# Kernel tuning notes

Measured on AMD Instinct MI355X. Metric: run time of the kernel, lower is better.

Reference implementation:

```python
import jax, jax.numpy as jnp
import numpy as np

D, H, L, NE, B, S, VOCAB = 512, 8, 4, 8, 32, 512, 64
HD = D // H
NEG = -1e9


def setup_inputs() -> dict:
    keys = iter(jax.random.split(jax.random.key(0), 64))
    def n(shape, s=0.02):
        return jax.random.normal(next(keys), shape, dtype=jnp.float32) * s
    return dict(
        x_batch=jax.random.randint(next(keys), (B, S), 0, VOCAB),
        context_batch=jax.random.normal(next(keys), (B, 2), dtype=jnp.float32),
        specialist_ids=jax.random.randint(next(keys), (B,), 0, NE),
        emb=n((VOCAB, D), 1.0),
        Wq=n((L, D, D)), bq=jnp.zeros((L, D)),
        Wk=n((L, D, D)), bk=jnp.zeros((L, D)),
        Wv=n((L, D, D)), bv=jnp.zeros((L, D)),
        Wo=n((L, D, D)), bo=jnp.zeros((L, D)),
        ln1_s=jnp.ones((L, D)), ln1_b=jnp.zeros((L, D)),
        ln2_s=jnp.ones((L, D)), ln2_b=jnp.zeros((L, D)),
        W1=n((L, D, 4 * D)), b1=jnp.zeros((L, 4 * D)),
        W2=n((L, 4 * D, D)), b2=jnp.zeros((L, D)),
        ctxW=n((2, D), 0.5), ctxb=jnp.zeros((D,)),
        cWq=n((D, D)), cbq=jnp.zeros((D,)),
        cWk=n((D, D)), cbk=jnp.zeros((D,)),
        cWv=n((D, D)), cbv=jnp.zeros((D,)),
        cWo=n((D, D)), cbo=jnp.zeros((D,)),
        spWp=n((NE, D, 64)), spbp=jnp.zeros((NE, 64)),
        spWa=n((NE, D, 64)), spba=jnp.zeros((NE, 64)),
    )


def _ln(x, s, b, eps=1e-5):
    m = x.mean(-1, keepdims=True)
    v = ((x - m) ** 2).mean(-1, keepdims=True)
    return (x - m) / jnp.sqrt(v + eps) * s + b


def _mha(q_in, kv_in, wq, bq_, wk, bk_, wv, bv_, wo, bo_, bias=None):
    # batch_first MultiheadAttention, H heads of dim HD
    Bq, Sq, _ = q_in.shape
    Sk = kv_in.shape[1]
    q = (q_in @ wq + bq_).reshape(Bq, Sq, H, HD).transpose(0, 2, 1, 3)
    k = (kv_in @ wk + bk_).reshape(Bq, Sk, H, HD).transpose(0, 2, 1, 3)
    v = (kv_in @ wv + bv_).reshape(Bq, Sk, H, HD).transpose(0, 2, 1, 3)
    scores = jnp.einsum('bhqd,bhkd->bhqk', q, k) / jnp.sqrt(jnp.float32(HD))
    if bias is not None:
        scores = scores + bias
    p = jax.nn.softmax(scores, axis=-1)
    o = jnp.einsum('bhqk,bhkd->bhqd', p, v).transpose(0, 2, 1, 3).reshape(Bq, Sq, D)
    return o @ wo + bo_


def reference(x_batch, context_batch, specialist_ids, emb, Wq, bq, Wk, bk, Wv, bv, Wo, bo,
              ln1_s, ln1_b, ln2_s, ln2_b, W1, b1, W2, b2, ctxW, ctxb,
              cWq, cbq, cWk, cbk, cWv, cbv, cWo, cbo, spWp, spbp, spWa, spba):
    x = emb[x_batch]  # [B,S,D]
    causal = jnp.where(jnp.tril(jnp.ones((S, S), dtype=bool)), 0.0, NEG)[None, None]
    # post-norm TransformerEncoderLayer (torch default): attn -> add+LN -> FFN(relu) -> add+LN
    for l in range(L):
        a = _mha(x, x, Wq[l], bq[l], Wk[l], bk[l], Wv[l], bv[l], Wo[l], bo[l], bias=causal)
        x = _ln(x + a, ln1_s[l], ln1_b[l])
        f = jax.nn.relu(x @ W1[l] + b1[l]) @ W2[l] + b2[l]
        x = _ln(x + f, ln2_s[l], ln2_b[l])
    ctx = (context_batch @ ctxW + ctxb)[:, None, :]  # [B,1,D]
    x = _mha(x, ctx, cWq, cbq, cWk, cbk, cWv, cbv, cWo, cbo)  # cross-attn, kv_len=1
    last = x[:, -1, :]  # [B,D]
    # expert routing: gather per-example expert params (equivalent to boolean-mask loop)
    pred = jnp.einsum('bd,bdo->bo', last, spWp[specialist_ids]) + spbp[specialist_ids]
    act = jnp.einsum('bd,bdo->bo', last, spWa[specialist_ids]) + spba[specialist_ids]
    return pred, act
```

## Files before the change

### kernel.cpp

```cpp
#include <hip/hip_runtime.h>


#define DD 512

__global__ __launch_bounds__(512) void stage_gemv3(
    const float* __restrict__ x0, const float* __restrict__ x1,
    const float* __restrict__ x2,
    const float* __restrict__ W,
    const float* __restrict__ bias2,
    float*       __restrict__ dst)
{
    __shared__ float sx[3 * DD];
    __shared__ float red[32][48];
    const int t = threadIdx.x;
    const int cbase = blockIdx.x * 16;

    if (t < DD) {
        sx[t]          = x0[t];
        sx[DD + t]     = x1[t];
        sx[2 * DD + t] = x2[t];
    }
    __syncthreads();

    const int c = t & 15, dg = t >> 4;
    const float* wp = W + (size_t)(dg * 16) * DD + cbase + c;
    float wreg[16];
    #pragma unroll
    for (int j = 0; j < 16; ++j)
        wreg[j] = wp[(size_t)j * DD];
    float p0 = 0.f, p1 = 0.f, p2 = 0.f;
    #pragma unroll
    for (int j = 0; j < 16; ++j) {
        const int d = dg * 16 + j;
        p0 += sx[d] * wreg[j];
        p1 += sx[DD + d] * wreg[j];
        p2 += sx[2 * DD + d] * wreg[j];
    }
    red[dg][c * 3 + 0] = p0;
    red[dg][c * 3 + 1] = p1;
    red[dg][c * 3 + 2] = p2;
    __syncthreads();

    if (t < 48) {
        const int cc = t / 3, vec = t % 3;
        float s = 0.f;
        #pragma unroll
        for (int g = 0; g < 32; ++g) s += red[g][t];
        if (vec == 2) s += bias2[cbase + cc];
        dst[vec * DD + cbase + cc] = s;
    }
}

__global__ __launch_bounds__(256) void stage_heads(
    const float* __restrict__ Bv,
    const float* __restrict__ spWp, const float* __restrict__ spbp,
    const float* __restrict__ spWa, const float* __restrict__ spba,
    const float* __restrict__ ctxin,
    const int*   __restrict__ sid,
    float*       __restrict__ out)
{
    __shared__ float sb[3 * DD];
    __shared__ float red[16][48];
    __shared__ float pv[48];
    __shared__ float sc0[32], sc1[32];
    __shared__ int   ssid[32];
    const int t = threadIdx.x;
    const int s = blockIdx.x & 7, h = (blockIdx.x >> 3) & 1, q = blockIdx.x >> 4;

    for (int i = t; i < 3 * DD; i += 256) sb[i] = Bv[i];
    if (t < 32) {
        ssid[t] = sid[t];
        sc0[t] = ctxin[2 * t];
        sc1[t] = ctxin[2 * t + 1];
    }
    __syncthreads();

    const float* W    = (h ? spWa : spWp) + (size_t)s * DD * 64;
    const float* bias = (h ? spba : spbp) + s * 64;
    const int o16 = t & 15, dg = t >> 4;
    const int o = q * 16 + o16;
    const float* wp = W + (size_t)(dg * 32) * 64 + o;
    float wreg[32];
    #pragma unroll
    for (int j = 0; j < 32; ++j)
        wreg[j] = wp[(size_t)j * 64];
    float p0 = 0.f, p1 = 0.f, p2 = 0.f;
    #pragma unroll
    for (int j = 0; j < 32; ++j) {
        const int d = dg * 32 + j;
        p0 += sb[d] * wreg[j];
        p1 += sb[DD + d] * wreg[j];
        p2 += sb[2 * DD + d] * wreg[j];
    }
    red[dg][o16 * 3 + 0] = p0;
    red[dg][o16 * 3 + 1] = p1;
    red[dg][o16 * 3 + 2] = p2;
    __syncthreads();

    if (t < 48) {
        const int oo = t / 3, vec = t % 3;
        float a = 0.f;
        #pragma unroll
        for (int g = 0; g < 16; ++g) a += red[g][t];
        if (vec == 2) a += bias[q * 16 + oo];
        pv[oo * 3 + vec] = a;
    }
    __syncthreads();

    if (t < 16) {
        const float v0 = pv[t * 3], v1 = pv[t * 3 + 1], v2 = pv[t * 3 + 2];
        #pragma unroll
        for (int b = 0; b < 32; ++b) {
            if (ssid[b] == s) {
                out[h * 2048 + b * 64 + q * 16 + t] =
                    sc0[b] * v0 + sc1[b] * v1 + v2;
            }
        }
    }
}

extern "C" void kernel_launch(void* const* d_in, const int* in_sizes, int n_in,
                              void* d_out, int out_size, void* d_ws, size_t ws_size,
                              hipStream_t stream) {
    const float* ctxin = (const float*)d_in[1];
    const int*   sid   = (const int*)d_in[2];
    const float* ctxW  = (const float*)d_in[20];
    const float* ctxb  = (const float*)d_in[21];
    const float* cWv   = (const float*)d_in[26];
    const float* cbv   = (const float*)d_in[27];
    const float* cWo   = (const float*)d_in[28];
    const float* cbo   = (const float*)d_in[29];
    const float* spWp  = (const float*)d_in[30];
    const float* spbp  = (const float*)d_in[31];
    const float* spWa  = (const float*)d_in[32];
    const float* spba  = (const float*)d_in[33];
    float* out = (float*)d_out;
    float* wsA = (float*)d_ws;
    float* wsB = wsA + 3 * DD;

    stage_gemv3<<<dim3(32), dim3(512), 0, stream>>>(
        ctxW, ctxW + DD, ctxb, cWv, cbv, wsA);
    stage_gemv3<<<dim3(32), dim3(512), 0, stream>>>(
        wsA, wsA + DD, wsA + 2 * DD, cWo, cbo, wsB);
    stage_heads<<<dim3(64), dim3(256), 0, stream>>>(
        wsB, spWp, spbp, spWa, spba, ctxin, sid, out);
}
```

Before: 152.3 us.

## Fuse three GEMV stages into one kernel with atomic accumulation and spin-wait

Replaces the three-kernel chain (value projection, output projection, expert heads) with one launch. Producer blocks compute the value projection and immediately apply their slice of the output projection, accumulating into a zeroed workspace with atomics and signalling a counter. Consumer blocks preload expert weights, spin on the counter, then finish the heads. This removes two kernel launches and lets weight loads overlap, at the cost of an extra memset, atomic contention, and reliance on all blocks being co-resident.

```diff
diff --git a/kernel.cpp b/kernel.cpp
--- a/kernel.cpp
+++ b/kernel.cpp
@@ -3,117 +3,165 @@
 
 #define DD 512
 
-__global__ __launch_bounds__(512) void stage_gemv3(
-    const float* __restrict__ x0, const float* __restrict__ x1,
-    const float* __restrict__ x2,
-    const float* __restrict__ W,
-    const float* __restrict__ bias2,
-    float*       __restrict__ dst)
-{
-    __shared__ float sx[3 * DD];
-    __shared__ float red[32][48];
-    const int t = threadIdx.x;
-    const int cbase = blockIdx.x * 16;
-
-    if (t < DD) {
-        sx[t]          = x0[t];
-        sx[DD + t]     = x1[t];
-        sx[2 * DD + t] = x2[t];
-    }
-    __syncthreads();
-
-    const int c = t & 15, dg = t >> 4;
-    const float* wp = W + (size_t)(dg * 16) * DD + cbase + c;
-    float wreg[16];
-    #pragma unroll
-    for (int j = 0; j < 16; ++j)
-        wreg[j] = wp[(size_t)j * DD];
-    float p0 = 0.f, p1 = 0.f, p2 = 0.f;
-    #pragma unroll
-    for (int j = 0; j < 16; ++j) {
-        const int d = dg * 16 + j;
-        p0 += sx[d] * wreg[j];
-        p1 += sx[DD + d] * wreg[j];
-        p2 += sx[2 * DD + d] * wreg[j];
-    }
-    red[dg][c * 3 + 0] = p0;
-    red[dg][c * 3 + 1] = p1;
-    red[dg][c * 3 + 2] = p2;
-    __syncthreads();
-
-    if (t < 48) {
-        const int cc = t / 3, vec = t % 3;
-        float s = 0.f;
-        #pragma unroll
-        for (int g = 0; g < 32; ++g) s += red[g][t];
-        if (vec == 2) s += bias2[cbase + cc];
-        dst[vec * DD + cbase + cc] = s;
-    }
-}
-
-__global__ __launch_bounds__(256) void stage_heads(
-    const float* __restrict__ Bv,
+__global__ __launch_bounds__(256) void fused_chain(
+    const float* __restrict__ ctxW,
+    const float* __restrict__ ctxb,
+    const float* __restrict__ cWv,
+    const float* __restrict__ cbv,
+    const float* __restrict__ cWo,
+    const float* __restrict__ cbo,
     const float* __restrict__ spWp, const float* __restrict__ spbp,
     const float* __restrict__ spWa, const float* __restrict__ spba,
     const float* __restrict__ ctxin,
     const int*   __restrict__ sid,
+    float*       __restrict__ Bacc,
+    unsigned*    __restrict__ ctr,
     float*       __restrict__ out)
 {
-    __shared__ float sb[3 * DD];
-    __shared__ float red[16][48];
-    __shared__ float pv[48];
-    __shared__ float sc0[32], sc1[32];
-    __shared__ int   ssid[32];
-    const int t = threadIdx.x;
-    const int s = blockIdx.x & 7, h = (blockIdx.x >> 3) & 1, q = blockIdx.x >> 4;
+    const int t   = threadIdx.x;
+    const int blk = blockIdx.x;
 
-    for (int i = t; i < 3 * DD; i += 256) sb[i] = Bv[i];
-    if (t < 32) {
-        ssid[t] = sid[t];
-        sc0[t] = ctxin[2 * t];
-        sc1[t] = ctxin[2 * t + 1];
-    }
-    __syncthreads();
+    if (blk < 32) {
+        __shared__ float sx[3 * DD];
+        __shared__ float red[16][48];
+        __shared__ float sA[48];
+        const int ebase = blk * 16;
+        const int e16 = t & 15, dg = t >> 4;
 
-    const float* W    = (h ? spWa : spWp) + (size_t)s * DD * 64;
-    const float* bias = (h ? spba : spbp) + s * 64;
-    const int o16 = t & 15, dg = t >> 4;
-    const int o = q * 16 + o16;
-    const float* wp = W + (size_t)(dg * 32) * 64 + o;
-    float wreg[32];
-    #pragma unroll
-    for (int j = 0; j < 32; ++j)
-        wreg[j] = wp[(size_t)j * 64];
-    float p0 = 0.f, p1 = 0.f, p2 = 0.f;
-    #pragma unroll
-    for (int j = 0; j < 32; ++j) {
-        const int d = dg * 32 + j;
-        p0 += sb[d] * wreg[j];
-        p1 += sb[DD + d] * wreg[j];
-        p2 += sb[2 * DD + d] * wreg[j];
-    }
-    red[dg][o16 * 3 + 0] = p0;
-    red[dg][o16 * 3 + 1] = p1;
-    red[dg][o16 * 3 + 2] = p2;
-    __syncthreads();
+        const float* wv = cWv + (size_t)(dg * 32) * DD + ebase + e16;
+        float wregV[32];
+        #pragma unroll
+        for (int j = 0; j < 32; ++j) wregV[j] = wv[(size_t)j * DD];
 
-    if (t < 48) {
-        const int oo = t / 3, vec = t % 3;
-        float a = 0.f;
+        const float* wo = cWo + (size_t)ebase * DD + t;
+        float wregO0[16], wregO1[16];
         #pragma unroll
-        for (int g = 0; g < 16; ++g) a += red[g][t];
-        if (vec == 2) a += bias[q * 16 + oo];
-        pv[oo * 3 + vec] = a;
-    }
-    __syncthreads();
+        for (int j = 0; j < 16; ++j) {
+            wregO0[j] = wo[(size_t)j * DD];
+            wregO1[j] = wo[(size_t)j * DD + 256];
+        }
 
-    if (t < 16) {
-        const float v0 = pv[t * 3], v1 = pv[t * 3 + 1], v2 = pv[t * 3 + 2];
+        for (int i = t; i < 2 * DD; i += 256) sx[i] = ctxW[i];
+        for (int i = t; i < DD; i += 256)     sx[2 * DD + i] = ctxb[i];
+        __syncthreads();
+
+        float p0 = 0.f, p1 = 0.f, p2 = 0.f;
         #pragma unroll
-        for (int b = 0; b < 32; ++b) {
-            if (ssid[b] == s) {
-                out[h * 2048 + b * 64 + q * 16 + t] =
-                    sc0[b] * v0 + sc1[b] * v1 + v2;
+        for (int j = 0; j < 32; ++j) {
+            const int d = dg * 32 + j;
+            p0 += sx[d] * wregV[j];
+            p1 += sx[DD + d] * wregV[j];
+            p2 += sx[2 * DD + d] * wregV[j];
+        }
+        red[dg][e16 * 3 + 0] = p0;
+        red[dg][e16 * 3 + 1] = p1;
+        red[dg][e16 * 3 + 2] = p2;
+        __syncthreads();
+
+        if (t < 48) {
+            float s = 0.f;
+            #pragma unroll
+            for (int g = 0; g < 16; ++g) s += red[g][t];
+            if (t % 3 == 2) s += cbv[ebase + t / 3];
+            sA[t] = s;
+        }
+        __syncthreads();
+
+        float b0a = 0.f, b1a = 0.f, b2a = 0.f;
+        float b0b = 0.f, b1b = 0.f, b2b = 0.f;
+        #pragma unroll
+        for (int j = 0; j < 16; ++j) {
+            const float a0 = sA[j * 3 + 0];
+            const float a1 = sA[j * 3 + 1];
+            const float a2 = sA[j * 3 + 2];
+            b0a += a0 * wregO0[j];  b1a += a1 * wregO0[j];  b2a += a2 * wregO0[j];
+            b0b += a0 * wregO1[j];  b1b += a1 * wregO1[j];  b2b += a2 * wregO1[j];
+        }
+        atomicAdd(&Bacc[0 * DD + t],       b0a);
+        atomicAdd(&Bacc[1 * DD + t],       b1a);
+        atomicAdd(&Bacc[2 * DD + t],       b2a);
+        atomicAdd(&Bacc[0 * DD + t + 256], b0b);
+        atomicAdd(&Bacc[1 * DD + t + 256], b1b);
+        atomicAdd(&Bacc[2 * DD + t + 256], b2b);
+        __syncthreads();
+        if (t == 0) {
+            __threadfence();
+            __hip_atomic_fetch_add(ctr, 1u, __ATOMIC_RELEASE,
+                                   __HIP_MEMORY_SCOPE_AGENT);
+        }
+    } else {
+        __shared__ float sb[3 * DD];
+        __shared__ float red[16][48];
+        __shared__ float pv[48];
+        __shared__ float sc0[32], sc1[32];
+        __shared__ int   ssid[32];
+        const int bb = blk - 32;
+        const int s = bb & 7, h = (bb >> 3) & 1, q = bb >> 4;
+
+        const float* W    = (h ? spWa : spWp) + (size_t)s * DD * 64;
+        const float* bias = (h ? spba : spbp) + s * 64;
+        const int o16 = t & 15, dg = t >> 4;
+        const float* wp = W + (size_t)(dg * 32) * 64 + q * 16 + o16;
+        float wreg[32];
+        #pragma unroll
+        for (int j = 0; j < 32; ++j) wreg[j] = wp[(size_t)j * 64];
+
+        if (t < 32) {
+            ssid[t] = sid[t];
+            sc0[t] = ctxin[2 * t];
+            sc1[t] = ctxin[2 * t + 1];
+        }
+
+        if (t < 64) {
+            for (int it = 0; it < (1 << 22); ++it) {
+                if (__hip_atomic_load(ctr, __ATOMIC_RELAXED,
+                                      __HIP_MEMORY_SCOPE_AGENT) == 32u)
+                    break;
+            }
+            __threadfence();
+        }
+        __syncthreads();
+
+        for (int i = t; i < 2 * DD; i += 256)
+            sb[i] = __hip_atomic_load(&Bacc[i], __ATOMIC_RELAXED,
+                                      __HIP_MEMORY_SCOPE_AGENT);
+        for (int i = t; i < DD; i += 256)
+            sb[2 * DD + i] = __hip_atomic_load(&Bacc[2 * DD + i],
+                                               __ATOMIC_RELAXED,
+                                               __HIP_MEMORY_SCOPE_AGENT)
+                             + cbo[i];
+        __syncthreads();
+
+        float p0 = 0.f, p1 = 0.f, p2 = 0.f;
+        #pragma unroll
+        for (int j = 0; j < 32; ++j) {
+            const int d = dg * 32 + j;
+            p0 += sb[d] * wreg[j];
+            p1 += sb[DD + d] * wreg[j];
+            p2 += sb[2 * DD + d] * wreg[j];
+        }
+        red[dg][o16 * 3 + 0] = p0;
+        red[dg][o16 * 3 + 1] = p1;
+        red[dg][o16 * 3 + 2] = p2;
+        __syncthreads();
+
+        if (t < 48) {
+            float a = 0.f;
+            #pragma unroll
+            for (int g = 0; g < 16; ++g) a += red[g][t];
+            if (t % 3 == 2) a += bias[q * 16 + t / 3];
+            pv[t] = a;
+        }
+        __syncthreads();
+
+        if (t < 16) {
+            const float v0 = pv[t * 3], v1 = pv[t * 3 + 1], v2 = pv[t * 3 + 2];
+            #pragma unroll
+            for (int b = 0; b < 32; ++b) {
+                if (ssid[b] == s) {
+                    out[h * 2048 + b * 64 + q * 16 + t] =
+                        sc0[b] * v0 + sc1[b] * v1 + v2;
+                }
             }
         }
     }
@@ -134,14 +182,13 @@
     const float* spbp  = (const float*)d_in[31];
     const float* spWa  = (const float*)d_in[32];
     const float* spba  = (const float*)d_in[33];
-    float* out = (float*)d_out;
-    float* wsA = (float*)d_ws;
-    float* wsB = wsA + 3 * DD;
+    float*    out  = (float*)d_out;
+    float*    Bacc = (float*)d_ws;
+    unsigned* ctr  = (unsigned*)((char*)d_ws + 3 * DD * sizeof(float));
 
-    stage_gemv3<<<dim3(32), dim3(512), 0, stream>>>(
-        ctxW, ctxW + DD, ctxb, cWv, cbv, wsA);
-    stage_gemv3<<<dim3(32), dim3(512), 0, stream>>>(
-        wsA, wsA + DD, wsA + 2 * DD, cWo, cbo, wsB);
-    stage_heads<<<dim3(64), dim3(256), 0, stream>>>(
-        wsB, spWp, spbp, spWa, spba, ctxin, sid, out);
+    hipMemsetAsync(d_ws, 0, 3 * DD * sizeof(float) + 64, stream);
+
+    fused_chain<<<dim3(96), dim3(256), 0, stream>>>(
+        ctxW, ctxb, cWv, cbv, cWo, cbo,
+        spWp, spbp, spWa, spba, ctxin, sid, Bacc, ctr, out);
 }
```

Result: no change. 153.3 us (+0.6%).
